# Performance work log

Measured on AMD Instinct MI355X. Metric: run time of the kernel, lower is better.

## Reference

```python
import jax, jax.numpy as jnp
import numpy as np

NEG_BIG = -9e15  # matches -9000000000000000.0 in the torch source
ALPHA = 0.2      # LeakyReLU slope


def setup_inputs() -> dict:
    key = jax.random.key(0)
    k1, k2, k3, k4 = jax.random.split(key, 4)
    N, F_in, F_out = 8192, 128, 64
    x = jax.random.normal(k1, (N, F_in), dtype=jnp.float32)
    adj = jax.random.normal(k2, (N, N), dtype=jnp.float32)
    W = jax.random.normal(k3, (F_in, F_out), dtype=jnp.float32) * 0.1
    a = jax.random.normal(k4, (2 * F_out,), dtype=jnp.float32) * 0.1
    return {"x": x, "adj": adj, "W": W, "a": a}


def reference(x, adj, W, a):
    F_out = W.shape[1]
    h = x @ W                      # [N, F_out]
    # a([h_i || h_j]) decomposes into a1.h_i + a2.h_j -> avoid the [N,N,2F] concat
    a1, a2 = a[:F_out], a[F_out:]
    s1 = h @ a1                    # [N] source scores
    s2 = h @ a2                    # [N] target scores
    e = jax.nn.leaky_relu(s1[:, None] + s2[None, :], negative_slope=ALPHA)  # [N, N]
    attention = jnp.where(adj > 0, e, NEG_BIG)
    attention = jax.nn.softmax(attention, axis=1)
    h_prime = attention @ h        # [N, F_out]
    return jax.nn.elu(h_prime)
```

## Files before the change

### kernel.cpp

```cpp
#include <hip/hip_runtime.h>
#include <hip/hip_bf16.h>

#define ALPHA 0.2f
#define NROW 8192

typedef __attribute__((ext_vector_type(4))) float f4;
typedef __attribute__((ext_vector_type(8))) short s8;

__device__ __forceinline__ short f2bf_bits(float x){
    __hip_bfloat16 b = __float2bfloat16(x);
    return __builtin_bit_cast(short, b);
}

__device__ __forceinline__ void gload_lds16(const void* g, void* l){
    __builtin_amdgcn_global_load_lds(
        (const __attribute__((address_space(1))) void*)g,
        (__attribute__((address_space(3))) void*)l, 16, 0, 0);
}

__global__ __launch_bounds__(256) void k_proj(
    const float* __restrict__ x, const float* __restrict__ W, const float* __restrict__ a,
    float* __restrict__ s1,
    float* __restrict__ F1, float* __restrict__ F2, __hip_bfloat16* __restrict__ hpack)
{
    __shared__ float Wsh[128*64];
    __shared__ float xsh[32*128];
    const int t = threadIdx.x;
    const int f = t & 63, wq = t >> 6;
    const int row0 = blockIdx.x * 32;
    for (int i = t; i < 128*64; i += 256) Wsh[i] = W[i];
    for (int i = t; i < 32*128; i += 256) xsh[i] = x[row0*128 + i];
    __syncthreads();
    const float a1 = a[f], a2 = a[64 + f];
    #pragma unroll 1
    for (int rr = 0; rr < 8; ++rr){
        const int ry = wq*8 + rr;
        float acc = 0.f;
        #pragma unroll
        for (int k = 0; k < 128; ++k) acc = fmaf(xsh[ry*128 + k], Wsh[k*64 + f], acc);
        float p1 = acc * a1, p2 = acc * a2;
        #pragma unroll
        for (int m = 32; m; m >>= 1){ p1 += __shfl_xor(p1, m, 64); p2 += __shfl_xor(p2, m, 64); }
        const int j = row0 + ry;
        if (f == 0){
            s1[j] = p1;
            F1[j] = __expf(p2); F2[j] = __expf(0.2f * p2);
        }
        const int sc = j >> 5, hg = (j >> 3) & 3, e = j & 7;
        const int fg = f >> 4, lr = f & 15;
        hpack[(((sc*4 + fg)*64) + hg*16 + lr)*8 + e] = __float2bfloat16(acc);
    }
}

__global__ __launch_bounds__(512, 2) void k_gat(
    const float* __restrict__ adj, const float* __restrict__ s1g,
    const float* __restrict__ F1g, const float* __restrict__ F2g,
    const __hip_bfloat16* __restrict__ hpack,
    float* __restrict__ part, float* __restrict__ pden)
{
    __shared__ __attribute__((aligned(16))) char arena[147456];

    const int tid = threadIdx.x;
    const int w = tid >> 6, lane = tid & 63;
    const int lr = lane & 15, hi = lane >> 4;
    const int jslab = blockIdx.x >> 6, igrp = blockIdx.x & 63;

    float* F1sl = (float*)(arena + 131072);
    float* F2sl = (float*)(arena + 139264);

    const int rbA = igrp*128 + w*16;
    const int row = rbA + lr;
    const float s1r = s1g[row];
    const float E1 = __expf(s1r), E2 = __expf(ALPHA*s1r), T1 = __expf(-s1r);

#define STAGEH(buf, sw_) do { \
    const s8* hp_ = (const s8*)hpack + (jslab*64 + (sw_)*16)*256 + w*512 + lane; \
    char* dst_ = arena + (buf)*65536 + (w*512)*16; \
    _Pragma("unroll") \
    for (int it_ = 0; it_ < 8; ++it_) \
        gload_lds16(hp_ + it_*64, dst_ + it_*1024); \
} while(0)

    STAGEH(0, 0);
    *(f4*)&F1sl[tid*4] = *(const f4*)(F1g + jslab*2048 + tid*4);
    *(f4*)&F2sl[tid*4] = *(const f4*)(F2g + jslab*2048 + tid*4);
    __syncthreads();

    const float* padj = adj + (long)(rbA + (lane >> 3))*NROW + jslab*2048 + (lane & 7)*4;
    const unsigned bsh = (unsigned)((lr & 7)*8 + hi*2);
    const int hi8 = hi * 8;

    f4 acc0={0,0,0,0}, acc1={0,0,0,0}, acc2={0,0,0,0}, acc3={0,0,0,0};
    float lsum = 0.f;

    f4 v0S0,v1S0, v0S1,v1S1, v0S2,v1S2, v0S3,v1S3;
    f4 v0S4,v1S4, v0S5,v1S5, v0S6,v1S6, v0S7,v1S7;

#define LOAD(S, s_) do { \
    const int o_ = (s_) * 32; \
    v0##S = *(const f4*)(padj + o_); \
    v1##S = *(const f4*)(padj + o_ + 8*NROW); \
} while(0)

#define CALCQ(cond, g1, g2, qd) { \
    float fz = ((g1) > T1) ? (g1) * E1 : (g2) * E2; \
    qd = (cond) ? fz : 0.f; }

#define STEP(S, s_) do { \
    unsigned long long c0_ = __ballot(v0##S[0] > 0.f); \
    unsigned long long c1_ = __ballot(v0##S[1] > 0.f); \
    unsigned long long c2_ = __ballot(v0##S[2] > 0.f); \
    unsigned long long c3_ = __ballot(v0##S[3] > 0.f); \
    unsigned long long d0_ = __ballot(v1##S[0] > 0.f); \
    unsigned long long d1_ = __ballot(v1##S[1] > 0.f); \
    unsigned long long d2_ = __ballot(v1##S[2] > 0.f); \
    unsigned long long d3_ = __ballot(v1##S[3] > 0.f); \
    const unsigned u0 = (unsigned)(((lr < 8) ? c0_ : d0_) >> bsh); \
    const unsigned u1 = (unsigned)(((lr < 8) ? c1_ : d1_) >> bsh); \
    const unsigned u2 = (unsigned)(((lr < 8) ? c2_ : d2_) >> bsh); \
    const unsigned u3 = (unsigned)(((lr < 8) ? c3_ : d3_) >> bsh); \
    const s8* hb_ = (const s8*)(arena + (((s_) >> 4) & 1)*65536) + ((s_) & 15)*256; \
    s8 h0 = hb_[lane]; s8 h1 = hb_[64 + lane]; \
    s8 h2 = hb_[128 + lane]; s8 h3 = hb_[192 + lane]; \
    f4 f1a = *(const f4*)&F1sl[(s_)*32 + hi8]; f4 f1b = *(const f4*)&F1sl[(s_)*32 + hi8 + 4]; \
    f4 f2a = *(const f4*)&F2sl[(s_)*32 + hi8]; f4 f2b = *(const f4*)&F2sl[(s_)*32 + hi8 + 4]; \
    float q0,q1,q2,q3,q4,q5,q6,q7; \
    CALCQ(u0 & 1u, f1a[0], f2a[0], q0); CALCQ(u1 & 1u, f1a[1], f2a[1], q1); \
    CALCQ(u2 & 1u, f1a[2], f2a[2], q2); CALCQ(u3 & 1u, f1a[3], f2a[3], q3); \
    CALCQ(u0 & 2u, f1b[0], f2b[0], q4); CALCQ(u1 & 2u, f1b[1], f2b[1], q5); \
    CALCQ(u2 & 2u, f1b[2], f2b[2], q6); CALCQ(u3 & 2u, f1b[3], f2b[3], q7); \
    lsum += ((q0+q1)+(q2+q3)) + ((q4+q5)+(q6+q7)); \
    s8 af; \
    af[0]=f2bf_bits(q0); af[1]=f2bf_bits(q1); af[2]=f2bf_bits(q2); af[3]=f2bf_bits(q3); \
    af[4]=f2bf_bits(q4); af[5]=f2bf_bits(q5); af[6]=f2bf_bits(q6); af[7]=f2bf_bits(q7); \
    acc0 = __builtin_amdgcn_mfma_f32_16x16x32_bf16(af, h0, acc0, 0, 0, 0); \
    acc1 = __builtin_amdgcn_mfma_f32_16x16x32_bf16(af, h1, acc1, 0, 0, 0); \
    acc2 = __builtin_amdgcn_mfma_f32_16x16x32_bf16(af, h2, acc2, 0, 0, 0); \
    acc3 = __builtin_amdgcn_mfma_f32_16x16x32_bf16(af, h3, acc3, 0, 0, 0); \
} while(0)

#define W14 asm volatile("s_waitcnt vmcnt(14)" ::: "memory")
#define ROUND8(stb) do { \
    W14; STEP(S0, (stb)    ); LOAD(S0, (stb) + 8); \
    W14; STEP(S1, (stb) + 1); LOAD(S1, (stb) + 9); \
    W14; STEP(S2, (stb) + 2); LOAD(S2, (stb) + 10); \
    W14; STEP(S3, (stb) + 3); LOAD(S3, (stb) + 11); \
    W14; STEP(S4, (stb) + 4); LOAD(S4, (stb) + 12); \
    W14; STEP(S5, (stb) + 5); LOAD(S5, (stb) + 13); \
    W14; STEP(S6, (stb) + 6); LOAD(S6, (stb) + 14); \
    W14; STEP(S7, (stb) + 7); LOAD(S7, (stb) + 15); \
} while(0)

    LOAD(S0, 0); LOAD(S1, 1); LOAD(S2, 2); LOAD(S3, 3);
    LOAD(S4, 4); LOAD(S5, 5); LOAD(S6, 6); LOAD(S7, 7);

    #pragma unroll 1
    for (int sw = 0; sw < 3; ++sw){
        STAGEH((sw + 1) & 1, sw + 1);
        const int stb = sw * 16;
        ROUND8(stb); ROUND8(stb + 8);
        asm volatile("s_barrier" ::: "memory");
    }
    ROUND8(48);
    W14;                                              STEP(S0, 56);
    asm volatile("s_waitcnt vmcnt(12)" ::: "memory"); STEP(S1, 57);
    asm volatile("s_waitcnt vmcnt(10)" ::: "memory"); STEP(S2, 58);
    asm volatile("s_waitcnt vmcnt(8)"  ::: "memory"); STEP(S3, 59);
    asm volatile("s_waitcnt vmcnt(6)"  ::: "memory"); STEP(S4, 60);
    asm volatile("s_waitcnt vmcnt(4)"  ::: "memory"); STEP(S5, 61);
    asm volatile("s_waitcnt vmcnt(2)"  ::: "memory"); STEP(S6, 62);
    asm volatile("s_waitcnt vmcnt(0)"  ::: "memory"); STEP(S7, 63);

#undef LOAD
#undef CALCQ
#undef STEP
#undef W14
#undef ROUND8
#undef STAGEH

    lsum += __shfl_xor(lsum, 16, 64);
    lsum += __shfl_xor(lsum, 32, 64);

    {
        const long pb = ((long)jslab*NROW + rbA + hi*4)*64 + lr;
        #pragma unroll
        for (int r = 0; r < 4; ++r){
            part[pb + r*64 +  0] = acc0[r];
            part[pb + r*64 + 16] = acc1[r];
            part[pb + r*64 + 32] = acc2[r];
            part[pb + r*64 + 48] = acc3[r];
        }
        if (lane < 16) pden[jslab*NROW + rbA + lr] = lsum;
    }
}

__global__ __launch_bounds__(256) void k_comb(
    const float* __restrict__ part, const float* __restrict__ pden,
    float* __restrict__ out)
{
    const int idx = blockIdx.x*256 + threadIdx.x;
    const int i = idx >> 4, c4 = (idx & 15) << 2;
    f4 sa = {0.f,0.f,0.f,0.f}; float L = 0.f;
    #pragma unroll
    for (int s = 0; s < 4; ++s){
        sa += *(const f4*)&part[((long)s*NROW + i)*64 + c4];
        L  += pden[s*NROW + i];
    }
    const float inv = 1.f / L;
    f4 o;
    #pragma unroll
    for (int e = 0; e < 4; ++e){
        float v = sa[e] * inv;
        o[e] = (v > 0.f) ? v : expm1f(v);
    }
    *(f4*)&out[(long)i*64 + c4] = o;
}

extern "C" void kernel_launch(void* const* d_in, const int* in_sizes, int n_in,
                              void* d_out, int out_size, void* d_ws, size_t ws_size,
                              hipStream_t stream)
{
    const float* x   = (const float*)d_in[0];
    const float* adj = (const float*)d_in[1];
    const float* W   = (const float*)d_in[2];
    const float* a   = (const float*)d_in[3];
    float* out = (float*)d_out;

    char* ws = (char*)d_ws;
    float* s1   = (float*)(ws);
    float* F1   = (float*)(ws + 65536);
    float* F2   = (float*)(ws + 98304);
    __hip_bfloat16* hpack = (__hip_bfloat16*)(ws + 131328);
    float* part = (float*)(ws + 1179904);
    float* pden = (float*)(ws + 9568512);

    k_proj <<<256, 256, 0, stream>>>(x, W, a, s1, F1, F2, hpack);
    k_gat  <<<256, 512, 0, stream>>>(adj, s1, F1, F2, hpack, part, pden);
    k_comb <<<512, 256, 0, stream>>>(part, pden, out);
}
```

Baseline: 67.63 us.

## Pack adjacency into per-wave LDS bitmasks with row-contiguous loads

```diff
diff --git a/kernel.cpp b/kernel.cpp
--- a/kernel.cpp
+++ b/kernel.cpp
@@ -58,7 +58,7 @@
     const __hip_bfloat16* __restrict__ hpack,
     float* __restrict__ part, float* __restrict__ pden)
 {
-    __shared__ __attribute__((aligned(16))) char arena[147456];
+    __shared__ __attribute__((aligned(16))) char arena[163840];
 
     const int tid = threadIdx.x;
     const int w = tid >> 6, lane = tid & 63;
@@ -67,11 +67,15 @@
 
     float* F1sl = (float*)(arena + 131072);
     float* F2sl = (float*)(arena + 139264);
+    char* wmask = arena + 147456 + w*2048;
 
     const int rbA = igrp*128 + w*16;
     const int row = rbA + lr;
     const float s1r = s1g[row];
     const float E1 = __expf(s1r), E2 = __expf(ALPHA*s1r), T1 = __expf(-s1r);
+    const int hi8 = hi * 8;
+
+    const float* psrc = adj + (long)rbA*NROW + jslab*2048 + lane*8;
 
 #define STAGEH(buf, sw_) do { \
     const s8* hp_ = (const s8*)hpack + (jslab*64 + (sw_)*16)*256 + w*512 + lane; \
@@ -81,54 +85,48 @@
         gload_lds16(hp_ + it_*64, dst_ + it_*1024); \
 } while(0)
 
-    STAGEH(0, 0);
-    *(f4*)&F1sl[tid*4] = *(const f4*)(F1g + jslab*2048 + tid*4);
-    *(f4*)&F2sl[tid*4] = *(const f4*)(F2g + jslab*2048 + tid*4);
-    __syncthreads();
-
-    const float* padj = adj + (long)(rbA + (lane >> 3))*NROW + jslab*2048 + (lane & 7)*4;
-    const unsigned bsh = (unsigned)((lr & 7)*8 + hi*2);
-    const int hi8 = hi * 8;
-
     f4 acc0={0,0,0,0}, acc1={0,0,0,0}, acc2={0,0,0,0}, acc3={0,0,0,0};
     float lsum = 0.f;
 
     f4 v0S0,v1S0, v0S1,v1S1, v0S2,v1S2, v0S3,v1S3;
     f4 v0S4,v1S4, v0S5,v1S5, v0S6,v1S6, v0S7,v1S7;
 
-#define LOAD(S, s_) do { \
-    const int o_ = (s_) * 32; \
-    v0##S = *(const f4*)(padj + o_); \
-    v1##S = *(const f4*)(padj + o_ + 8*NROW); \
+#define LOADR(S, r_, swp_) do { \
+    const float* p_ = psrc + (long)(r_)*NROW + (swp_)*512; \
+    v0##S = *(const f4*)(p_); v1##S = *(const f4*)(p_ + 4); \
 } while(0)
+
+#define PRODR(S, r_, swp_) do { \
+    unsigned bb = 0; \
+    bb |= (v0##S[0] > 0.f) ?   1u : 0u; bb |= (v0##S[1] > 0.f) ?   2u : 0u; \
+    bb |= (v0##S[2] > 0.f) ?   4u : 0u; bb |= (v0##S[3] > 0.f) ?   8u : 0u; \
+    bb |= (v1##S[0] > 0.f) ?  16u : 0u; bb |= (v1##S[1] > 0.f) ?  32u : 0u; \
+    bb |= (v1##S[2] > 0.f) ?  64u : 0u; bb |= (v1##S[3] > 0.f) ? 128u : 0u; \
+    unsigned tt = bb | (__shfl_xor(bb, 1) << 8); \
+    tt |= (__shfl_xor(tt, 2) << 16); \
+    if ((lane & 3) == 0){ \
+        *(unsigned*)(wmask + ((swp_)&1)*1024 + (r_)*64 + \
+            ((((lane>>2) ^ (((r_)>>1)&7)))<<2)) = tt; \
+    } } while(0)
 
 #define CALCQ(cond, g1, g2, qd) { \
     float fz = ((g1) > T1) ? (g1) * E1 : (g2) * E2; \
     qd = (cond) ? fz : 0.f; }
 
-#define STEP(S, s_) do { \
-    unsigned long long c0_ = __ballot(v0##S[0] > 0.f); \
-    unsigned long long c1_ = __ballot(v0##S[1] > 0.f); \
-    unsigned long long c2_ = __ballot(v0##S[2] > 0.f); \
-    unsigned long long c3_ = __ballot(v0##S[3] > 0.f); \
-    unsigned long long d0_ = __ballot(v1##S[0] > 0.f); \
-    unsigned long long d1_ = __ballot(v1##S[1] > 0.f); \
-    unsigned long long d2_ = __ballot(v1##S[2] > 0.f); \
-    unsigned long long d3_ = __ballot(v1##S[3] > 0.f); \
-    const unsigned u0 = (unsigned)(((lr < 8) ? c0_ : d0_) >> bsh); \
-    const unsigned u1 = (unsigned)(((lr < 8) ? c1_ : d1_) >> bsh); \
-    const unsigned u2 = (unsigned)(((lr < 8) ? c2_ : d2_) >> bsh); \
-    const unsigned u3 = (unsigned)(((lr < 8) ? c3_ : d3_) >> bsh); \
-    const s8* hb_ = (const s8*)(arena + (((s_) >> 4) & 1)*65536) + ((s_) & 15)*256; \
+#define CONS(st_) do { \
+    const int s_ = (st_) & 15, cb_ = ((st_) >> 4) & 1; \
+    unsigned mb = *(const unsigned char*)(wmask + cb_*1024 + lr*64 + \
+        (((s_) ^ ((lr>>1)&7))<<2) + hi); \
+    const s8* hb_ = (const s8*)(arena + cb_*65536) + s_*256; \
     s8 h0 = hb_[lane]; s8 h1 = hb_[64 + lane]; \
     s8 h2 = hb_[128 + lane]; s8 h3 = hb_[192 + lane]; \
-    f4 f1a = *(const f4*)&F1sl[(s_)*32 + hi8]; f4 f1b = *(const f4*)&F1sl[(s_)*32 + hi8 + 4]; \
-    f4 f2a = *(const f4*)&F2sl[(s_)*32 + hi8]; f4 f2b = *(const f4*)&F2sl[(s_)*32 + hi8 + 4]; \
+    f4 f1a = *(const f4*)&F1sl[(st_)*32 + hi8]; f4 f1b = *(const f4*)&F1sl[(st_)*32 + hi8 + 4]; \
+    f4 f2a = *(const f4*)&F2sl[(st_)*32 + hi8]; f4 f2b = *(const f4*)&F2sl[(st_)*32 + hi8 + 4]; \
     float q0,q1,q2,q3,q4,q5,q6,q7; \
-    CALCQ(u0 & 1u, f1a[0], f2a[0], q0); CALCQ(u1 & 1u, f1a[1], f2a[1], q1); \
-    CALCQ(u2 & 1u, f1a[2], f2a[2], q2); CALCQ(u3 & 1u, f1a[3], f2a[3], q3); \
-    CALCQ(u0 & 2u, f1b[0], f2b[0], q4); CALCQ(u1 & 2u, f1b[1], f2b[1], q5); \
-    CALCQ(u2 & 2u, f1b[2], f2b[2], q6); CALCQ(u3 & 2u, f1b[3], f2b[3], q7); \
+    CALCQ(mb &   1u, f1a[0], f2a[0], q0); CALCQ(mb &   2u, f1a[1], f2a[1], q1); \
+    CALCQ(mb &   4u, f1a[2], f2a[2], q2); CALCQ(mb &   8u, f1a[3], f2a[3], q3); \
+    CALCQ(mb &  16u, f1b[0], f2b[0], q4); CALCQ(mb &  32u, f1b[1], f2b[1], q5); \
+    CALCQ(mb &  64u, f1b[2], f2b[2], q6); CALCQ(mb & 128u, f1b[3], f2b[3], q7); \
     lsum += ((q0+q1)+(q2+q3)) + ((q4+q5)+(q6+q7)); \
     s8 af; \
     af[0]=f2bf_bits(q0); af[1]=f2bf_bits(q1); af[2]=f2bf_bits(q2); af[3]=f2bf_bits(q3); \
@@ -139,44 +137,76 @@
     acc3 = __builtin_amdgcn_mfma_f32_16x16x32_bf16(af, h3, acc3, 0, 0, 0); \
 } while(0)
 
-#define W14 asm volatile("s_waitcnt vmcnt(14)" ::: "memory")
-#define ROUND8(stb) do { \
-    W14; STEP(S0, (stb)    ); LOAD(S0, (stb) + 8); \
-    W14; STEP(S1, (stb) + 1); LOAD(S1, (stb) + 9); \
-    W14; STEP(S2, (stb) + 2); LOAD(S2, (stb) + 10); \
-    W14; STEP(S3, (stb) + 3); LOAD(S3, (stb) + 11); \
-    W14; STEP(S4, (stb) + 4); LOAD(S4, (stb) + 12); \
-    W14; STEP(S5, (stb) + 5); LOAD(S5, (stb) + 13); \
-    W14; STEP(S6, (stb) + 6); LOAD(S6, (stb) + 14); \
-    W14; STEP(S7, (stb) + 7); LOAD(S7, (stb) + 15); \
-} while(0)
-
-    LOAD(S0, 0); LOAD(S1, 1); LOAD(S2, 2); LOAD(S3, 3);
-    LOAD(S4, 4); LOAD(S5, 5); LOAD(S6, 6); LOAD(S7, 7);
-
-    #pragma unroll 1
-    for (int sw = 0; sw < 3; ++sw){
-        STAGEH((sw + 1) & 1, sw + 1);
-        const int stb = sw * 16;
-        ROUND8(stb); ROUND8(stb + 8);
-        asm volatile("s_barrier" ::: "memory");
-    }
-    ROUND8(48);
-    W14;                                              STEP(S0, 56);
-    asm volatile("s_waitcnt vmcnt(12)" ::: "memory"); STEP(S1, 57);
-    asm volatile("s_waitcnt vmcnt(10)" ::: "memory"); STEP(S2, 58);
-    asm volatile("s_waitcnt vmcnt(8)"  ::: "memory"); STEP(S3, 59);
-    asm volatile("s_waitcnt vmcnt(6)"  ::: "memory"); STEP(S4, 60);
-    asm volatile("s_waitcnt vmcnt(4)"  ::: "memory"); STEP(S5, 61);
-    asm volatile("s_waitcnt vmcnt(2)"  ::: "memory"); STEP(S6, 62);
-    asm volatile("s_waitcnt vmcnt(0)"  ::: "memory"); STEP(S7, 63);
-
-#undef LOAD
+#define WN(n) asm volatile("s_waitcnt vmcnt(" #n ")" ::: "memory")
+#define BAR do { asm volatile("s_waitcnt lgkmcnt(0)" ::: "memory"); \
+                 __builtin_amdgcn_s_barrier(); } while(0)
+
+#define LOADU(S, u_) LOADR(S, (u_) & 15, ((u_) >> 4) + 1)
+#define PRODU(S, u_) PRODR(S, (u_) & 15, ((u_) >> 4) + 1)
+#define STEPA(S, g_) do { WN(22); PRODU(S, g_); LOADU(S, (g_) + 8); CONS(g_); } while(0)
+#define STEPB(S, g_) do { WN(14); PRODU(S, g_); LOADU(S, (g_) + 8); CONS(g_); } while(0)
+#define STEPT(S, g_, n_) do { WN(n_); PRODU(S, g_); CONS(g_); } while(0)
+
+    *(f4*)&F1sl[tid*4] = *(const f4*)(F1g + jslab*2048 + tid*4);
+    *(f4*)&F2sl[tid*4] = *(const f4*)(F2g + jslab*2048 + tid*4);
+    STAGEH(0, 0);
+    LOADR(S0,0,0); LOADR(S1,1,0); LOADR(S2,2,0); LOADR(S3,3,0);
+    LOADR(S4,4,0); LOADR(S5,5,0); LOADR(S6,6,0); LOADR(S7,7,0);
+    WN(14); PRODR(S0,0,0); LOADR(S0, 8,0);
+    WN(14); PRODR(S1,1,0); LOADR(S1, 9,0);
+    WN(14); PRODR(S2,2,0); LOADR(S2,10,0);
+    WN(14); PRODR(S3,3,0); LOADR(S3,11,0);
+    WN(14); PRODR(S4,4,0); LOADR(S4,12,0);
+    WN(14); PRODR(S5,5,0); LOADR(S5,13,0);
+    WN(14); PRODR(S6,6,0); LOADR(S6,14,0);
+    WN(14); PRODR(S7,7,0); LOADR(S7,15,0);
+    WN(14); PRODR(S0, 8,0);
+    WN(12); PRODR(S1, 9,0);
+    WN(10); PRODR(S2,10,0);
+    WN(8);  PRODR(S3,11,0);
+    WN(6);  PRODR(S4,12,0);
+    WN(4);  PRODR(S5,13,0);
+    WN(2);  PRODR(S6,14,0);
+    WN(0);  PRODR(S7,15,0);
+    LOADR(S0,0,1); LOADR(S1,1,1); LOADR(S2,2,1); LOADR(S3,3,1);
+    LOADR(S4,4,1); LOADR(S5,5,1); LOADR(S6,6,1); LOADR(S7,7,1);
+    BAR;
+
+    STAGEH(1, 1);
+    STEPA(S0, 0); STEPA(S1, 1); STEPA(S2, 2); STEPA(S3, 3);
+    STEPA(S4, 4); STEPA(S5, 5); STEPA(S6, 6); STEPA(S7, 7);
+    STEPB(S0, 8); STEPB(S1, 9); STEPB(S2,10); STEPB(S3,11);
+    STEPB(S4,12); STEPB(S5,13); STEPB(S6,14); STEPB(S7,15);
+    BAR;
+    STAGEH(0, 2);
+    STEPA(S0,16); STEPA(S1,17); STEPA(S2,18); STEPA(S3,19);
+    STEPA(S4,20); STEPA(S5,21); STEPA(S6,22); STEPA(S7,23);
+    STEPB(S0,24); STEPB(S1,25); STEPB(S2,26); STEPB(S3,27);
+    STEPB(S4,28); STEPB(S5,29); STEPB(S6,30); STEPB(S7,31);
+    BAR;
+    STAGEH(1, 3);
+    STEPA(S0,32); STEPA(S1,33); STEPA(S2,34); STEPA(S3,35);
+    STEPA(S4,36); STEPA(S5,37); STEPA(S6,38); STEPA(S7,39);
+    STEPT(S0,40,14); STEPT(S1,41,12); STEPT(S2,42,10); STEPT(S3,43,8);
+    STEPT(S4,44,6);  STEPT(S5,45,4);  STEPT(S6,46,2);  STEPT(S7,47,0);
+    BAR;
+    CONS(48); CONS(49); CONS(50); CONS(51);
+    CONS(52); CONS(53); CONS(54); CONS(55);
+    CONS(56); CONS(57); CONS(58); CONS(59);
+    CONS(60); CONS(61); CONS(62); CONS(63);
+
+#undef STAGEH
+#undef LOADR
+#undef PRODR
 #undef CALCQ
-#undef STEP
-#undef W14
-#undef ROUND8
-#undef STAGEH
+#undef CONS
+#undef WN
+#undef BAR
+#undef LOADU
+#undef PRODU
+#undef STEPA
+#undef STEPB
+#undef STEPT
 
     lsum += __shfl_xor(lsum, 16, 64);
     lsum += __shfl_xor(lsum, 32, 64);
```

Result: slower. 219.5 us (+224.5%).

## Shrink GAT block to 4 waves with smaller LDS stages for higher occupancy

Applied to the files above, without the earlier changes.

```diff
diff --git a/kernel.cpp b/kernel.cpp
--- a/kernel.cpp
+++ b/kernel.cpp
@@ -52,43 +52,38 @@
     }
 }
 
-__global__ __launch_bounds__(512, 2) void k_gat(
+__global__ __launch_bounds__(256, 2) void k_gat(
     const float* __restrict__ adj, const float* __restrict__ s1g,
     const float* __restrict__ F1g, const float* __restrict__ F2g,
     const __hip_bfloat16* __restrict__ hpack,
     float* __restrict__ part, float* __restrict__ pden)
 {
-    __shared__ __attribute__((aligned(16))) char arena[147456];
+    __shared__ __attribute__((aligned(16))) char arena[81920];
 
     const int tid = threadIdx.x;
     const int w = tid >> 6, lane = tid & 63;
     const int lr = lane & 15, hi = lane >> 4;
-    const int jslab = blockIdx.x >> 6, igrp = blockIdx.x & 63;
-
-    float* F1sl = (float*)(arena + 131072);
-    float* F2sl = (float*)(arena + 139264);
-
-    const int rbA = igrp*128 + w*16;
+    const int jslab = blockIdx.x >> 7, igrp = blockIdx.x & 127;
+
+    float* F1sl = (float*)(arena + 65536);
+    float* F2sl = (float*)(arena + 73728);
+
+    const int rbA = igrp*64 + w*16;
     const int row = rbA + lr;
     const float s1r = s1g[row];
     const float E1 = __expf(s1r), E2 = __expf(ALPHA*s1r), T1 = __expf(-s1r);
+    const int hi8 = hi * 8;
 
 #define STAGEH(buf, sw_) do { \
-    const s8* hp_ = (const s8*)hpack + (jslab*64 + (sw_)*16)*256 + w*512 + lane; \
-    char* dst_ = arena + (buf)*65536 + (w*512)*16; \
+    const s8* hp_ = (const s8*)hpack + (jslab*64 + (sw_)*8)*256 + w*512 + lane; \
+    char* dst_ = arena + (buf)*32768 + w*8192; \
     _Pragma("unroll") \
     for (int it_ = 0; it_ < 8; ++it_) \
         gload_lds16(hp_ + it_*64, dst_ + it_*1024); \
 } while(0)
 
-    STAGEH(0, 0);
-    *(f4*)&F1sl[tid*4] = *(const f4*)(F1g + jslab*2048 + tid*4);
-    *(f4*)&F2sl[tid*4] = *(const f4*)(F2g + jslab*2048 + tid*4);
-    __syncthreads();
-
     const float* padj = adj + (long)(rbA + (lane >> 3))*NROW + jslab*2048 + (lane & 7)*4;
     const unsigned bsh = (unsigned)((lr & 7)*8 + hi*2);
-    const int hi8 = hi * 8;
 
     f4 acc0={0,0,0,0}, acc1={0,0,0,0}, acc2={0,0,0,0}, acc3={0,0,0,0};
     float lsum = 0.f;
@@ -119,7 +114,7 @@
     const unsigned u1 = (unsigned)(((lr < 8) ? c1_ : d1_) >> bsh); \
     const unsigned u2 = (unsigned)(((lr < 8) ? c2_ : d2_) >> bsh); \
     const unsigned u3 = (unsigned)(((lr < 8) ? c3_ : d3_) >> bsh); \
-    const s8* hb_ = (const s8*)(arena + (((s_) >> 4) & 1)*65536) + ((s_) & 15)*256; \
+    const s8* hb_ = (const s8*)(arena + (((s_) >> 3) & 1)*32768) + ((s_) & 7)*256; \
     s8 h0 = hb_[lane]; s8 h1 = hb_[64 + lane]; \
     s8 h2 = hb_[128 + lane]; s8 h3 = hb_[192 + lane]; \
     f4 f1a = *(const f4*)&F1sl[(s_)*32 + hi8]; f4 f1b = *(const f4*)&F1sl[(s_)*32 + hi8 + 4]; \
@@ -139,29 +134,34 @@
     acc3 = __builtin_amdgcn_mfma_f32_16x16x32_bf16(af, h3, acc3, 0, 0, 0); \
 } while(0)
 
+#define W22 asm volatile("s_waitcnt vmcnt(22)" ::: "memory")
 #define W14 asm volatile("s_waitcnt vmcnt(14)" ::: "memory")
-#define ROUND8(stb) do { \
-    W14; STEP(S0, (stb)    ); LOAD(S0, (stb) + 8); \
-    W14; STEP(S1, (stb) + 1); LOAD(S1, (stb) + 9); \
-    W14; STEP(S2, (stb) + 2); LOAD(S2, (stb) + 10); \
-    W14; STEP(S3, (stb) + 3); LOAD(S3, (stb) + 11); \
-    W14; STEP(S4, (stb) + 4); LOAD(S4, (stb) + 12); \
-    W14; STEP(S5, (stb) + 5); LOAD(S5, (stb) + 13); \
-    W14; STEP(S6, (stb) + 6); LOAD(S6, (stb) + 14); \
-    W14; STEP(S7, (stb) + 7); LOAD(S7, (stb) + 15); \
-} while(0)
-
+#define BAR do { asm volatile("s_waitcnt lgkmcnt(0)" ::: "memory"); \
+                 __builtin_amdgcn_s_barrier(); } while(0)
+
+    STAGEH(0, 0);
+    *(f4*)&F1sl[tid*8]     = *(const f4*)(F1g + jslab*2048 + tid*8);
+    *(f4*)&F1sl[tid*8 + 4] = *(const f4*)(F1g + jslab*2048 + tid*8 + 4);
+    *(f4*)&F2sl[tid*8]     = *(const f4*)(F2g + jslab*2048 + tid*8);
+    *(f4*)&F2sl[tid*8 + 4] = *(const f4*)(F2g + jslab*2048 + tid*8 + 4);
     LOAD(S0, 0); LOAD(S1, 1); LOAD(S2, 2); LOAD(S3, 3);
     LOAD(S4, 4); LOAD(S5, 5); LOAD(S6, 6); LOAD(S7, 7);
+    __syncthreads();
 
     #pragma unroll 1
-    for (int sw = 0; sw < 3; ++sw){
+    for (int sw = 0; sw < 7; ++sw){
+        const int st = sw * 8;
         STAGEH((sw + 1) & 1, sw + 1);
-        const int stb = sw * 16;
-        ROUND8(stb); ROUND8(stb + 8);
-        asm volatile("s_barrier" ::: "memory");
-    }
-    ROUND8(48);
+        W22; STEP(S0, st    ); LOAD(S0, st + 8);
+        W22; STEP(S1, st + 1); LOAD(S1, st + 9);
+        W22; STEP(S2, st + 2); LOAD(S2, st + 10);
+        W22; STEP(S3, st + 3); LOAD(S3, st + 11);
+        W14; STEP(S4, st + 4); LOAD(S4, st + 12);
+        W14; STEP(S5, st + 5); LOAD(S5, st + 13);
+        W14; STEP(S6, st + 6); LOAD(S6, st + 14);
+        W14; STEP(S7, st + 7); LOAD(S7, st + 15);
+        BAR;
+    }
     W14;                                              STEP(S0, 56);
     asm volatile("s_waitcnt vmcnt(12)" ::: "memory"); STEP(S1, 57);
     asm volatile("s_waitcnt vmcnt(10)" ::: "memory"); STEP(S2, 58);
@@ -171,12 +171,13 @@
     asm volatile("s_waitcnt vmcnt(2)"  ::: "memory"); STEP(S6, 62);
     asm volatile("s_waitcnt vmcnt(0)"  ::: "memory"); STEP(S7, 63);
 
+#undef STAGEH
 #undef LOAD
 #undef CALCQ
 #undef STEP
+#undef W22
 #undef W14
-#undef ROUND8
-#undef STAGEH
+#undef BAR
 
     lsum += __shfl_xor(lsum, 16, 64);
     lsum += __shfl_xor(lsum, 32, 64);
@@ -235,6 +236,6 @@
     float* pden = (float*)(ws + 9568512);
 
     k_proj <<<256, 256, 0, stream>>>(x, W, a, s1, F1, F2, hpack);
-    k_gat  <<<256, 512, 0, stream>>>(adj, s1, F1, F2, hpack, part, pden);
+    k_gat  <<<512, 256, 0, stream>>>(adj, s1, F1, F2, hpack, part, pden);
     k_comb <<<512, 256, 0, stream>>>(part, pden, out);
 }
```

New measurement: 100.2 us. +48.2%, slower.
